# Kernel tuning notes

Hardware: AMD Instinct MI355X
Metric: run time of the kernel (lower is better)

The kernel has to match this reference:

```python
import jax, jax.numpy as jnp
import numpy as np

D = 768
H = 8
HD = D // H
FF = 4 * D


def _linear_params(key, din, dout):
    kw, kb = jax.random.split(key)
    lim = 1.0 / np.sqrt(din)
    W = jax.random.uniform(kw, (din, dout), jnp.float32, -lim, lim)
    b = jax.random.uniform(kb, (dout,), jnp.float32, -lim, lim)
    return W, b


def setup_inputs() -> dict:
    key = jax.random.key(0)
    ks = jax.random.split(key, 8)
    x = jax.random.normal(ks[0], (16, 1024, D), jnp.float32)
    Wq, bq = _linear_params(ks[1], D, D)
    Wk, bk = _linear_params(ks[2], D, D)
    Wv, bv = _linear_params(ks[3], D, D)
    Wo, bo = _linear_params(ks[4], D, D)
    W1, b1 = _linear_params(ks[5], D, FF)
    W2, b2 = _linear_params(ks[6], FF, D)
    gamma = jnp.ones((D,), jnp.float32)
    beta = jnp.zeros((D,), jnp.float32)
    return {"x": x, "gamma": gamma, "beta": beta,
            "Wq": Wq, "bq": bq, "Wk": Wk, "bk": bk, "Wv": Wv, "bv": bv,
            "Wo": Wo, "bo": bo, "W1": W1, "b1": b1, "W2": W2, "b2": b2}


def _layernorm(x, gamma, beta, eps=1e-5):
    mu = jnp.mean(x, axis=-1, keepdims=True)
    var = jnp.var(x, axis=-1, keepdims=True)
    return (x - mu) * jax.lax.rsqrt(var + eps) * gamma + beta


def _block(x, gamma, beta, Wq, bq, Wk, bk, Wv, bv, Wo, bo, W1, b1, W2, b2):
    b, n, d = x.shape
    residual = x
    h = _layernorm(x, gamma, beta)
    # QKV projections -> [b, h, n, hd]
    q = (h @ Wq + bq).reshape(b, n, H, HD).transpose(0, 2, 1, 3)
    k = (h @ Wk + bk).reshape(b, n, H, HD).transpose(0, 2, 1, 3)
    v = (h @ Wv + bv).reshape(b, n, H, HD).transpose(0, 2, 1, 3)
    scale = HD ** 0.5
    scores = jnp.einsum('bhid,bhjd->bhij', q, k) / scale
    attn = jax.nn.softmax(scores, axis=-1)
    out = jnp.einsum('bhij,bhjd->bhid', attn, v)
    out = out.transpose(0, 2, 1, 3).reshape(b, n, d)
    out = out @ Wo + bo
    out = out + residual
    residual = out
    h = _layernorm(out, gamma, beta)  # same LN params reused (as in source)
    h = jax.nn.gelu(h @ W1 + b1, approximate=False)
    h = h @ W2 + b2
    return h + residual


def reference(x, gamma, beta, Wq, bq, Wk, bk, Wv, bv, Wo, bo, W1, b1, W2, b2):
    return _block(x, gamma, beta, Wq, bq, Wk, bk, Wv, bv, Wo, bo, W1, b1, W2, b2)
```

## Files before the change

kernel.cpp:

```cpp
#include <hip/hip_runtime.h>

typedef unsigned short u16;
typedef float f32x4 __attribute__((ext_vector_type(4)));
typedef __bf16 bf16x8 __attribute__((ext_vector_type(8)));

#define AS1 __attribute__((address_space(1)))
#define AS3 __attribute__((address_space(3)))

__device__ __forceinline__ float bf2f(u16 h) {
  return __uint_as_float(((unsigned)h) << 16);
}
__device__ __forceinline__ u16 f2bf(float f) {
  unsigned u = __float_as_uint(f);
  unsigned r = (u + 0x7FFFu + ((u >> 16) & 1u)) >> 16;
  return (u16)r;
}
__device__ __forceinline__ void gload16(const u16* g, u16* l) {
  __builtin_amdgcn_global_load_lds((const AS1 void*)g, (AS3 void*)l, 16, 0, 0);
}

__global__ void transpose_k(const float* __restrict__ in, u16* __restrict__ out,
                            int R, int C) {
  __shared__ u16 t[32][33];
  int c0 = blockIdx.x * 32, r0 = blockIdx.y * 32;
  int tx = threadIdx.x & 31, ty = threadIdx.x >> 5;
  for (int i = 0; i < 32; i += 8)
    t[ty + i][tx] = f2bf(in[(size_t)(r0 + ty + i) * C + c0 + tx]);
  __syncthreads();
  for (int i = 0; i < 32; i += 8)
    out[(size_t)(c0 + ty + i) * R + r0 + tx] = t[tx][ty + i];
}

__global__ void vtrans_k(const u16* __restrict__ v, u16* __restrict__ vt) {
  __shared__ u16 t[32][33];
  int bh = blockIdx.z, b = bh >> 3, h = bh & 7;
  int n0 = blockIdx.y * 32, d0 = blockIdx.x * 32;
  int tx = threadIdx.x & 31, ty = threadIdx.x >> 5;
  const u16* src = v + (size_t)(b * 1024) * 768 + h * 96;
  for (int i = 0; i < 32; i += 8)
    t[ty + i][tx] = src[(size_t)(n0 + ty + i) * 768 + d0 + tx];
  __syncthreads();
  u16* dst = vt + ((size_t)bh * 96 + d0) * 1024 + n0;
  for (int i = 0; i < 32; i += 8)
    dst[(size_t)(ty + i) * 1024 + tx] = t[tx][ty + i];
}

__global__ __launch_bounds__(256) void ln_f32_k(const float* __restrict__ x,
                                                const float* __restrict__ gamma,
                                                const float* __restrict__ beta,
                                                u16* __restrict__ out) {
  __shared__ float red[8];
  int row = blockIdx.x, t = threadIdx.x;
  const float* xr = x + (size_t)row * 768;
  float v[3], s = 0.f, s2 = 0.f;
#pragma unroll
  for (int i = 0; i < 3; i++) {
    v[i] = xr[t + i * 256];
    s += v[i]; s2 += v[i] * v[i];
  }
#pragma unroll
  for (int off = 1; off < 64; off <<= 1) {
    s += __shfl_xor(s, off, 64);
    s2 += __shfl_xor(s2, off, 64);
  }
  int w = t >> 6;
  if ((t & 63) == 0) { red[w] = s; red[4 + w] = s2; }
  __syncthreads();
  s = red[0] + red[1] + red[2] + red[3];
  s2 = red[4] + red[5] + red[6] + red[7];
  float mu = s * (1.f / 768.f);
  float var = s2 * (1.f / 768.f) - mu * mu;
  float rs = rsqrtf(var + 1e-5f);
  u16* orow = out + (size_t)row * 768;
#pragma unroll
  for (int i = 0; i < 3; i++) {
    int c = t + i * 256;
    orow[c] = f2bf((v[i] - mu) * rs * gamma[c] + beta[c]);
  }
}

#define BM 128
#define BN 128
#define BK 32

template <int EPI>
__global__ __launch_bounds__(256, 2) void gemm_bt(
    const u16* __restrict__ A, const u16* __restrict__ Bt,
    const float* __restrict__ bias, const float* __restrict__ res,
    void* __restrict__ Cv, int M, int N, int K) {
  __shared__ u16 As[BM * BK];
  __shared__ u16 Bs[BN * BK];
  int tid = threadIdx.x, lane = tid & 63, w = tid >> 6;
  int l15 = lane & 15, quad = lane >> 4;
  int wm = (w >> 1) * 64, wn = (w & 1) * 64;
  int m0 = blockIdx.x * BM, n0 = blockIdx.y * BN;
  f32x4 acc[4][4] = {};
  for (int k0 = 0; k0 < K; k0 += BK) {
    __syncthreads();
#pragma unroll
    for (int i = 0; i < 2; i++) {
      int c = w * 2 + i;
      int e = c * 512 + lane * 8;
      int r = e >> 5, col = e & 31;
      gload16(A + (size_t)(m0 + r) * K + k0 + col, As + c * 512);
      gload16(Bt + (size_t)(n0 + r) * K + k0 + col, Bs + c * 512);
    }
    __syncthreads();
    bf16x8 af[4], bfv[4];
#pragma unroll
    for (int i = 0; i < 4; i++) {
      af[i] = *(const bf16x8*)(As + (wm + i * 16 + l15) * BK + quad * 8);
      bfv[i] = *(const bf16x8*)(Bs + (wn + i * 16 + l15) * BK + quad * 8);
    }
#pragma unroll
    for (int mt = 0; mt < 4; mt++)
#pragma unroll
      for (int nt = 0; nt < 4; nt++)
        acc[mt][nt] = __builtin_amdgcn_mfma_f32_16x16x32_bf16(
            af[mt], bfv[nt], acc[mt][nt], 0, 0, 0);
  }
#pragma unroll
  for (int nt = 0; nt < 4; nt++) {
    int col = n0 + wn + nt * 16 + l15;
    float bv = bias[col];
#pragma unroll
    for (int mt = 0; mt < 4; mt++) {
      int row = m0 + wm + mt * 16 + quad * 4;
#pragma unroll
      for (int r = 0; r < 4; r++) {
        float v = acc[mt][nt][r] + bv;
        size_t idx = (size_t)(row + r) * N + col;
        if (EPI == 4) {
          v += res[idx];
          ((float*)Cv)[idx] = v;
        } else {
          if (EPI == 2) v = 0.5f * v * (1.0f + erff(v * 0.70710678118654752f));
          ((u16*)Cv)[idx] = f2bf(v);
        }
      }
    }
  }
}

#define QSS 104
#define VSS 72
#define PSS 72
__global__ __launch_bounds__(256, 2) void attn_k(const u16* __restrict__ q,
                                                 const u16* __restrict__ k,
                                                 const u16* __restrict__ vt,
                                                 u16* __restrict__ o) {
  __shared__ u16 qs[64 * QSS];
  __shared__ u16 ks[2][64 * QSS];
  __shared__ u16 vts[2][96 * VSS];
  __shared__ u16 ps[4 * 16 * PSS];
  int tid = threadIdx.x, lane = tid & 63, w = tid >> 6;
  int l15 = lane & 15, quad = lane >> 4;
  int qt = blockIdx.x, bh = blockIdx.y;
  int b = bh >> 3, h = bh & 7;
  const u16* qbase = q + (size_t)(b * 1024 + qt * 64) * 768 + h * 96;
  const u16* kbase = k + (size_t)(b * 1024) * 768 + h * 96;
  const u16* vtbase = vt + (size_t)bh * 96 * 1024;
  int kr[3], ko[3], vr[3], vo[3];
#pragma unroll
  for (int i = 0; i < 3; i++) {
    int c = tid + i * 256;
    kr[i] = c / 12; ko[i] = (c % 12) * 8;
    vr[i] = c >> 3; vo[i] = (c & 7) * 8;
  }
#pragma unroll
  for (int i = 0; i < 3; i++)
    *(uint4*)(qs + kr[i] * QSS + ko[i]) =
        *(const uint4*)(qbase + (size_t)kr[i] * 768 + ko[i]);
  uint4 kreg[3], vreg[3];
#pragma unroll
  for (int i = 0; i < 3; i++) {
    kreg[i] = *(const uint4*)(kbase + (size_t)kr[i] * 768 + ko[i]);
    vreg[i] = *(const uint4*)(vtbase + (size_t)vr[i] * 1024 + vo[i]);
  }
#pragma unroll
  for (int i = 0; i < 3; i++) {
    *(uint4*)(ks[0] + kr[i] * QSS + ko[i]) = kreg[i];
    *(uint4*)(vts[0] + vr[i] * VSS + vo[i]) = vreg[i];
  }
  __syncthreads();

  float mi[4], li[4];
#pragma unroll
  for (int r = 0; r < 4; r++) { mi[r] = -1e30f; li[r] = 0.f; }
  f32x4 oacc[6] = {};
  const float scale = 0.10206207261596577f;
  for (int kt = 0; kt < 16; kt++) {
    int cur = kt & 1, nxt = cur ^ 1;
    int ktn = (kt + 1) & 15;
#pragma unroll
    for (int i = 0; i < 3; i++) {
      kreg[i] = *(const uint4*)(kbase + (size_t)(ktn * 64 + kr[i]) * 768 + ko[i]);
      vreg[i] = *(const uint4*)(vtbase + (size_t)vr[i] * 1024 + ktn * 64 + vo[i]);
    }
    f32x4 s[4] = {};
#pragma unroll
    for (int kk = 0; kk < 3; kk++) {
      bf16x8 a = *(const bf16x8*)(qs + (w * 16 + l15) * QSS + kk * 32 + quad * 8);
#pragma unroll
      for (int nt = 0; nt < 4; nt++) {
        bf16x8 bb =
            *(const bf16x8*)(ks[cur] + (nt * 16 + l15) * QSS + kk * 32 + quad * 8);
        s[nt] = __builtin_amdgcn_mfma_f32_16x16x32_bf16(a, bb, s[nt], 0, 0, 0);
      }
    }
#pragma unroll
    for (int r = 0; r < 4; r++) {
      float sv[4], mx = -1e30f;
#pragma unroll
      for (int nt = 0; nt < 4; nt++) {
        sv[nt] = s[nt][r] * scale;
        mx = fmaxf(mx, sv[nt]);
      }
#pragma unroll
      for (int off = 1; off < 16; off <<= 1) mx = fmaxf(mx, __shfl_xor(mx, off, 16));
      float mnew = fmaxf(mi[r], mx);
      float alpha = __expf(mi[r] - mnew);
      float rs = 0.f;
#pragma unroll
      for (int nt = 0; nt < 4; nt++) { sv[nt] = __expf(sv[nt] - mnew); rs += sv[nt]; }
#pragma unroll
      for (int off = 1; off < 16; off <<= 1) rs += __shfl_xor(rs, off, 16);
      li[r] = li[r] * alpha + rs;
      mi[r] = mnew;
#pragma unroll
      for (int ht = 0; ht < 6; ht++) oacc[ht][r] *= alpha;
      int prow = quad * 4 + r;
#pragma unroll
      for (int nt = 0; nt < 4; nt++)
        ps[w * 16 * PSS + prow * PSS + nt * 16 + l15] = f2bf(sv[nt]);
    }
    asm volatile("s_waitcnt lgkmcnt(0)" ::: "memory");
#pragma unroll
    for (int kk = 0; kk < 2; kk++) {
      bf16x8 a = *(const bf16x8*)(ps + w * 16 * PSS + l15 * PSS + kk * 32 + quad * 8);
#pragma unroll
      for (int ht = 0; ht < 6; ht++) {
        bf16x8 bb =
            *(const bf16x8*)(vts[cur] + (ht * 16 + l15) * VSS + kk * 32 + quad * 8);
        oacc[ht] = __builtin_amdgcn_mfma_f32_16x16x32_bf16(a, bb, oacc[ht], 0, 0, 0);
      }
    }
#pragma unroll
    for (int i = 0; i < 3; i++) {
      *(uint4*)(ks[nxt] + kr[i] * QSS + ko[i]) = kreg[i];
      *(uint4*)(vts[nxt] + vr[i] * VSS + vo[i]) = vreg[i];
    }
    __syncthreads();
  }
  u16* obase = o + (size_t)(b * 1024 + qt * 64 + w * 16) * 768 + h * 96;
#pragma unroll
  for (int r = 0; r < 4; r++) {
    float inv = 1.0f / li[r];
    int row = quad * 4 + r;
#pragma unroll
    for (int ht = 0; ht < 6; ht++)
      obase[(size_t)row * 768 + ht * 16 + l15] = f2bf(oacc[ht][r] * inv);
  }
}

extern "C" void kernel_launch(void* const* d_in, const int* in_sizes, int n_in,
                              void* d_out, int out_size, void* d_ws,
                              size_t ws_size, hipStream_t stream) {
  const float* x = (const float*)d_in[0];
  const float* gamma = (const float*)d_in[1];
  const float* beta = (const float*)d_in[2];
  const float* Wq = (const float*)d_in[3];
  const float* bq = (const float*)d_in[4];
  const float* Wk = (const float*)d_in[5];
  const float* bk = (const float*)d_in[6];
  const float* Wv = (const float*)d_in[7];
  const float* bv = (const float*)d_in[8];
  const float* Wo = (const float*)d_in[9];
  const float* bo = (const float*)d_in[10];
  const float* W1 = (const float*)d_in[11];
  const float* b1 = (const float*)d_in[12];
  const float* W2 = (const float*)d_in[13];
  const float* b2 = (const float*)d_in[14];
  float* out = (float*)d_out;

  char* ws = (char*)d_ws;
  size_t off = 0;
  auto alloc = [&](size_t elems) {
    u16* p = (u16*)(ws + off);
    off += elems * sizeof(u16);
    return p;
  };
  u16* WqT = alloc(768 * 768);
  u16* WkT = alloc(768 * 768);
  u16* WvT = alloc(768 * 768);
  u16* WoT = alloc(768 * 768);
  u16* W1T = alloc((size_t)768 * 3072);
  u16* W2T = alloc((size_t)3072 * 768);
  u16* hb = alloc((size_t)16384 * 768);
  u16* qb = alloc((size_t)16384 * 768);
  u16* kb = alloc((size_t)16384 * 768);
  u16* vb = alloc((size_t)16384 * 768);

  transpose_k<<<dim3(24, 24), 256, 0, stream>>>(Wq, WqT, 768, 768);
  transpose_k<<<dim3(24, 24), 256, 0, stream>>>(Wk, WkT, 768, 768);
  transpose_k<<<dim3(24, 24), 256, 0, stream>>>(Wv, WvT, 768, 768);
  transpose_k<<<dim3(24, 24), 256, 0, stream>>>(Wo, WoT, 768, 768);
  transpose_k<<<dim3(96, 24), 256, 0, stream>>>(W1, W1T, 768, 3072);
  transpose_k<<<dim3(24, 96), 256, 0, stream>>>(W2, W2T, 3072, 768);

  ln_f32_k<<<16384, 256, 0, stream>>>(x, gamma, beta, hb);
  gemm_bt<0><<<dim3(128, 6), 256, 0, stream>>>(hb, WqT, bq, nullptr, qb,
                                               16384, 768, 768);
  gemm_bt<0><<<dim3(128, 6), 256, 0, stream>>>(hb, WkT, bk, nullptr, kb,
                                               16384, 768, 768);
  gemm_bt<0><<<dim3(128, 6), 256, 0, stream>>>(hb, WvT, bv, nullptr, vb,
                                               16384, 768, 768);
  vtrans_k<<<dim3(3, 32, 128), 256, 0, stream>>>(vb, hb);
  attn_k<<<dim3(16, 128), 256, 0, stream>>>(qb, kb, hb, vb);
  gemm_bt<4><<<dim3(128, 6), 256, 0, stream>>>(vb, WoT, bo, x, out,
                                               16384, 768, 768);
  ln_f32_k<<<16384, 256, 0, stream>>>(out, gamma, beta, kb);
  for (int c = 0; c < 4; c++) {
    const u16* h2c = kb + (size_t)c * 4096 * 768;
    const float* y1c = out + (size_t)c * 4096 * 768;
    float* outc = out + (size_t)c * 4096 * 768;
    gemm_bt<2><<<dim3(32, 24), 256, 0, stream>>>(h2c, W1T, b1, nullptr, vb,
                                                 4096, 3072, 768);
    gemm_bt<4><<<dim3(32, 6), 256, 0, stream>>>(vb, W2T, b2, y1c, outc,
                                                4096, 768, 3072);
  }
}
```

Baseline: 858.2 us.

## Double GEMM K-tile with swizzled LDS, XCD-aware block remap, defer softmax row-sum reduction

Measured after the change: 820.7 us. 4.4% less time.

```diff
diff --git a/kernel.cpp b/kernel.cpp
--- a/kernel.cpp
+++ b/kernel.cpp
@@ -81,7 +81,7 @@
 
 #define BM 128
 #define BN 128
-#define BK 32
+#define BK 64
 
 template <int EPI>
 __global__ __launch_bounds__(256, 2) void gemm_bt(
@@ -93,31 +93,41 @@
   int tid = threadIdx.x, lane = tid & 63, w = tid >> 6;
   int l15 = lane & 15, quad = lane >> 4;
   int wm = (w >> 1) * 64, wn = (w & 1) * 64;
-  int m0 = blockIdx.x * BM, n0 = blockIdx.y * BN;
+  int GX = gridDim.x;
+  int f = blockIdx.y * GX + blockIdx.x;
+  int mpx = GX >> 3;
+  int xcd = f & 7, idx = f >> 3;
+  int m0 = (xcd * mpx + (idx % mpx)) * BM;
+  int n0 = (idx / mpx) * BN;
+  int srow = lane >> 3;
+  int scol = ((lane & 7) ^ srow) * 8;
   f32x4 acc[4][4] = {};
   for (int k0 = 0; k0 < K; k0 += BK) {
     __syncthreads();
 #pragma unroll
-    for (int i = 0; i < 2; i++) {
-      int c = w * 2 + i;
-      int e = c * 512 + lane * 8;
-      int r = e >> 5, col = e & 31;
-      gload16(A + (size_t)(m0 + r) * K + k0 + col, As + c * 512);
-      gload16(Bt + (size_t)(n0 + r) * K + k0 + col, Bs + c * 512);
+    for (int i = 0; i < 4; i++) {
+      int c = w * 4 + i;
+      int r = c * 8 + srow;
+      gload16(A + (size_t)(m0 + r) * K + k0 + scol, As + c * 512);
+      gload16(Bt + (size_t)(n0 + r) * K + k0 + scol, Bs + c * 512);
     }
     __syncthreads();
-    bf16x8 af[4], bfv[4];
-#pragma unroll
-    for (int i = 0; i < 4; i++) {
-      af[i] = *(const bf16x8*)(As + (wm + i * 16 + l15) * BK + quad * 8);
-      bfv[i] = *(const bf16x8*)(Bs + (wn + i * 16 + l15) * BK + quad * 8);
-    }
-#pragma unroll
-    for (int mt = 0; mt < 4; mt++)
-#pragma unroll
-      for (int nt = 0; nt < 4; nt++)
-        acc[mt][nt] = __builtin_amdgcn_mfma_f32_16x16x32_bf16(
-            af[mt], bfv[nt], acc[mt][nt], 0, 0, 0);
+#pragma unroll
+    for (int kk = 0; kk < 2; kk++) {
+      bf16x8 af[4], bfv[4];
+      int sa = ((kk * 4 + quad) ^ (l15 & 7)) * 8;
+#pragma unroll
+      for (int i = 0; i < 4; i++) {
+        af[i] = *(const bf16x8*)(As + (wm + i * 16 + l15) * BK + sa);
+        bfv[i] = *(const bf16x8*)(Bs + (wn + i * 16 + l15) * BK + sa);
+      }
+#pragma unroll
+      for (int mt = 0; mt < 4; mt++)
+#pragma unroll
+        for (int nt = 0; nt < 4; nt++)
+          acc[mt][nt] = __builtin_amdgcn_mfma_f32_16x16x32_bf16(
+              af[mt], bfv[nt], acc[mt][nt], 0, 0, 0);
+    }
   }
 #pragma unroll
   for (int nt = 0; nt < 4; nt++) {
@@ -129,13 +139,13 @@
 #pragma unroll
       for (int r = 0; r < 4; r++) {
         float v = acc[mt][nt][r] + bv;
-        size_t idx = (size_t)(row + r) * N + col;
+        size_t idx2 = (size_t)(row + r) * N + col;
         if (EPI == 4) {
-          v += res[idx];
-          ((float*)Cv)[idx] = v;
+          v += res[idx2];
+          ((float*)Cv)[idx2] = v;
         } else {
           if (EPI == 2) v = 0.5f * v * (1.0f + erff(v * 0.70710678118654752f));
-          ((u16*)Cv)[idx] = f2bf(v);
+          ((u16*)Cv)[idx2] = f2bf(v);
         }
       }
     }
@@ -155,7 +165,12 @@
   __shared__ u16 ps[4 * 16 * PSS];
   int tid = threadIdx.x, lane = tid & 63, w = tid >> 6;
   int l15 = lane & 15, quad = lane >> 4;
-  int qt = blockIdx.x, bh = blockIdx.y;
+  {
+  }
+  int f = blockIdx.y * 16 + blockIdx.x;
+  int xcd = f & 7, idx = f >> 3;
+  int bh = xcd * 16 + (idx & 15);
+  int qt = idx >> 4;
   int b = bh >> 3, h = bh & 7;
   const u16* qbase = q + (size_t)(b * 1024 + qt * 64) * 768 + h * 96;
   const u16* kbase = k + (size_t)(b * 1024) * 768 + h * 96;
@@ -213,18 +228,19 @@
       float sv[4], mx = -1e30f;
 #pragma unroll
       for (int nt = 0; nt < 4; nt++) {
-        sv[nt] = s[nt][r] * scale;
+        sv[nt] = s[nt][r];
         mx = fmaxf(mx, sv[nt]);
       }
 #pragma unroll
       for (int off = 1; off < 16; off <<= 1) mx = fmaxf(mx, __shfl_xor(mx, off, 16));
       float mnew = fmaxf(mi[r], mx);
-      float alpha = __expf(mi[r] - mnew);
+      float alpha = __expf((mi[r] - mnew) * scale);
       float rs = 0.f;
 #pragma unroll
-      for (int nt = 0; nt < 4; nt++) { sv[nt] = __expf(sv[nt] - mnew); rs += sv[nt]; }
-#pragma unroll
-      for (int off = 1; off < 16; off <<= 1) rs += __shfl_xor(rs, off, 16);
+      for (int nt = 0; nt < 4; nt++) {
+        sv[nt] = __expf((sv[nt] - mnew) * scale);
+        rs += sv[nt];
+      }
       li[r] = li[r] * alpha + rs;
       mi[r] = mnew;
 #pragma unroll
@@ -252,6 +268,10 @@
     }
     __syncthreads();
   }
+#pragma unroll
+  for (int r = 0; r < 4; r++)
+#pragma unroll
+    for (int off = 1; off < 16; off <<= 1) li[r] += __shfl_xor(li[r], off, 16);
   u16* obase = o + (size_t)(b * 1024 + qt * 64 + w * 16) * 768 + h * 96;
 #pragma unroll
   for (int r = 0; r < 4; r++) {
```
